# Performance work log

Measured on AMD Instinct MI355X. Metric: run time of the kernel, lower is better.

Reference implementation:

```python
import jax, jax.numpy as jnp
import numpy as np

D_MODEL = 1024
NHEAD = 16
HEAD_DIM = D_MODEL // NHEAD
MASK_FILLER = -1e20


def setup_inputs() -> dict:
    key = jax.random.key(0)
    ks = jax.random.split(key, 8)
    B, S = 2, 2048
    query = jax.random.normal(ks[0], (B, S, D_MODEL), dtype=jnp.float32)
    key_t = jax.random.normal(ks[1], (B, S, D_MODEL), dtype=jnp.float32)
    value = jax.random.normal(ks[2], (B, S, D_MODEL), dtype=jnp.float32)
    mask = jax.random.randint(ks[3], (B, S, S), 0, 2, dtype=jnp.int32)
    # nn.Linear(d_model, d_model, bias=False) weights, shape [out, in]
    scale = 1.0 / np.sqrt(D_MODEL)
    wq = jax.random.uniform(ks[4], (D_MODEL, D_MODEL), jnp.float32, -scale, scale)
    wk = jax.random.uniform(ks[5], (D_MODEL, D_MODEL), jnp.float32, -scale, scale)
    wv = jax.random.uniform(ks[6], (D_MODEL, D_MODEL), jnp.float32, -scale, scale)
    wo = jax.random.uniform(ks[7], (D_MODEL, D_MODEL), jnp.float32, -scale, scale)
    return {"query": query, "key": key_t, "value": value, "mask": mask,
            "wq": wq, "wk": wk, "wv": wv, "wo": wo}


def reference(query, key, value, mask, wq, wk, wv, wo):
    B = query.shape[0]
    # Projections: nn.Linear -> x @ W.T
    q = (query @ wq.T).reshape(B, -1, NHEAD, HEAD_DIM).transpose(0, 2, 1, 3)  # [B,H,Sq,Dh]
    k = (key @ wk.T).reshape(B, -1, NHEAD, HEAD_DIM).transpose(0, 2, 1, 3)    # [B,H,Sk,Dh]
    v = (value @ wv.T).reshape(B, -1, NHEAD, HEAD_DIM).transpose(0, 2, 1, 3)  # [B,H,Sk,Dh]
    scores = jnp.einsum('bhqd,bhkd->bhqk', q, k) / jnp.sqrt(jnp.float32(HEAD_DIM))
    scores = jnp.where(mask[:, None, :, :] == 0, MASK_FILLER, scores)
    attn = jax.nn.softmax(scores, axis=-1)  # dropout p=0.0 -> identity
    out = jnp.einsum('bhqk,bhkd->bhqd', attn, v)  # [B,H,Sq,Dh]
    out = out.transpose(0, 2, 1, 3).reshape(B, -1, D_MODEL)
    return out @ wo.T
```

## Files before the change

kernel.cpp:

```cpp
#include <hip/hip_runtime.h>
#include <stdint.h>

typedef __bf16 bf16x8 __attribute__((ext_vector_type(8)));
typedef float floatx4 __attribute__((ext_vector_type(4)));
typedef unsigned short ushort8v __attribute__((ext_vector_type(8)));
typedef unsigned int uint4v __attribute__((ext_vector_type(4)));
typedef unsigned short u16;
typedef unsigned long long u64;

#define GLOAD_LDS16(gp, lp)                                                       \
  __builtin_amdgcn_global_load_lds((__attribute__((address_space(1))) void*)(gp), \
                                   (__attribute__((address_space(3))) void*)(lp), \
                                   16, 0, 0)

__device__ __forceinline__ u16 f2bf(float f) {
  uint32_t u = __builtin_bit_cast(uint32_t, f);
  u = (u + 0x7FFFu + ((u >> 16) & 1u)) >> 16;
  return (u16)u;
}
__device__ __forceinline__ u16 f2bf_up(float f) {
  return (u16)((__builtin_bit_cast(uint32_t, f) + 0x8000u) >> 16);
}

__device__ __forceinline__ ushort8v load8(const void* base, size_t elemOff, int isf32) {
  if (isf32) {
    const uint32_t* p = (const uint32_t*)base + elemOff;
    uint4v a = *(const uint4v*)p;
    uint4v b = *(const uint4v*)(p + 4);
#pragma unroll
    for (int i = 0; i < 4; ++i) { a[i] += 0x8000u; b[i] += 0x8000u; }
    uint4v r;
    r[0] = __builtin_amdgcn_perm(a[1], a[0], 0x07060302);
    r[1] = __builtin_amdgcn_perm(a[3], a[2], 0x07060302);
    r[2] = __builtin_amdgcn_perm(b[1], b[0], 0x07060302);
    r[3] = __builtin_amdgcn_perm(b[3], b[2], 0x07060302);
    return __builtin_bit_cast(ushort8v, r);
  }
  return *(const ushort8v*)((const u16*)base + elemOff);
}

__global__ void detect_dtype(const u16* __restrict__ q, int* __restrict__ flag) {
  if (threadIdx.x == 0) *flag = 0;
  __syncthreads();
  int hit = 0;
  for (int i = threadIdx.x; i < 8192; i += 256) {
    u16 u = q[i];
    if (((u >> 7) & 0xFF) == 0xFF) hit = 1;
  }
  if (hit) atomicOr(flag, 1);
}

__global__ void pack_mask(const int* __restrict__ mask, u64* __restrict__ mpk) {
  const int gw   = (blockIdx.x * 256 + threadIdx.x) >> 6;
  const int lane = threadIdx.x & 63;
  const int word = gw & 31;
  const int row  = gw >> 5;
  const int m = mask[(size_t)row * 2048 + word * 64 + lane];
  u64 bits = __ballot(m != 0);
  if (lane == 0) mpk[(size_t)row * 32 + word] = bits;
}

__global__ __launch_bounds__(256)
void cvt_all(const void* X0, const void* X1, const void* X2,
             const void* W0, const void* W1, const void* W2, const void* W3,
             u16* __restrict__ Xb, u16* __restrict__ Wb, const int* flagp)
{
  const int isf = *flagp;
  const int id = blockIdx.x;
  const int t  = threadIdx.x;
  const int r2  = t >> 7;
  const int col = (t & 127) * 8;
  const void* src; u16* dst; int row;
  if (id < 6144) {
    const int s = id >> 11;
    src = (s == 0) ? X0 : (s == 1) ? X1 : X2;
    row = (id & 2047) * 2 + r2;
    dst = Xb + (size_t)s * 4096 * 1040 + (size_t)row * 1040 + col;
  } else {
    const int s = (id - 6144) >> 9;
    src = (s == 0) ? W0 : (s == 1) ? W1 : (s == 2) ? W2 : W3;
    row = ((id - 6144) & 511) * 2 + r2;
    dst = Wb + (size_t)s * 1024 * 1040 + (size_t)row * 1040 + col;
  }
  *(ushort8v*)dst = load8(src, (size_t)row * 1024 + col, isf);
}

__global__ __launch_bounds__(256)
void cvt_w(const void* W0, const void* W1, const void* W2, const void* W3,
           u16* __restrict__ dst, const int* flagp) {
  const int isf = *flagp;
  const int z = blockIdx.y;
  const void* src = (z == 0) ? W0 : (z == 1) ? W1 : (z == 2) ? W2 : W3;
  const size_t off = ((size_t)blockIdx.x * 256 + threadIdx.x) * 8;
  *(ushort8v*)(dst + (size_t)z * 1024 * 1024 + off) = load8(src, off, isf);
}

__global__ __launch_bounds__(256, 3)
void gemm_qkv_b(const u16* __restrict__ Xb, const u16* __restrict__ Wb,
                u16* __restrict__ Qb, u16* __restrict__ Kb, u16* __restrict__ Vt)
{
  const int AS = 1040, WS = 1040, N = 1024, K = 1024;
  const int z = blockIdx.z;
  const u16* A = Xb + (size_t)z * 4096 * AS;
  const u16* W = Wb + (size_t)z * 1024 * WS;

  __shared__ __align__(16) u16 lA[2 * 128 * 32];
  __shared__ __align__(16) u16 lB[2 * 128 * 32];

  const int tid  = threadIdx.x;
  const int lane = tid & 63;
  const int quad = lane >> 4;
  const int l15  = lane & 15;
  const int w    = tid >> 6;
  const int wm   = w >> 1, wn = w & 1;
  const int tileM = blockIdx.x * 128;
  const int tileN = blockIdx.y * 128;

  floatx4 acc[4][4] = {};

  const int ldRow = tid >> 2;
  const int ldCol = (tid & 3) * 8;
  const u16* aG = A + (size_t)(tileM + ldRow) * AS + ldCol;
  const u16* bG = W + (size_t)(tileN + ldRow) * WS + ldCol;
  u16* lAp = lA + tid * 8;
  u16* lBp = lB + tid * 8;

  GLOAD_LDS16(aG, lAp);
  GLOAD_LDS16(aG + (size_t)64 * AS, lAp + 2048);
  GLOAD_LDS16(bG, lBp);
  GLOAD_LDS16(bG + (size_t)64 * WS, lBp + 2048);
  __syncthreads();

#pragma unroll 2
  for (int k0 = 0; k0 < K; k0 += 32) {
    const int cur = (k0 >> 5) & 1;
    const int nxo = 4096 * (cur ^ 1);
    if (k0 + 32 < K) {
      GLOAD_LDS16(aG + k0 + 32, lAp + nxo);
      GLOAD_LDS16(aG + (size_t)64 * AS + k0 + 32, lAp + nxo + 2048);
      GLOAD_LDS16(bG + k0 + 32, lBp + nxo);
      GLOAD_LDS16(bG + (size_t)64 * WS + k0 + 32, lBp + nxo + 2048);
    }
    const u16* cA = lA + 4096 * cur;
    const u16* cB = lB + 4096 * cur;
    bf16x8 af[4], bw[4];
#pragma unroll
    for (int i = 0; i < 4; ++i) {
      af[i] = *(const bf16x8*)&cA[(wm * 64 + i * 16 + l15) * 32 + quad * 8];
      bw[i] = *(const bf16x8*)&cB[(wn * 64 + i * 16 + l15) * 32 + quad * 8];
    }
#pragma unroll
    for (int i = 0; i < 4; ++i)
#pragma unroll
      for (int j = 0; j < 4; ++j)
        acc[i][j] = __builtin_amdgcn_mfma_f32_16x16x32_bf16(af[i], bw[j], acc[i][j], 0, 0, 0);
    __syncthreads();
  }

  if (z < 2) {
    u16* C = (z == 0) ? Qb : Kb;
    const float sc = (z == 0) ? 0.18033688011112042f : 1.0f;
#pragma unroll
    for (int i = 0; i < 4; ++i) {
      const int row0 = tileM + wm * 64 + i * 16 + quad * 4;
#pragma unroll
      for (int j = 0; j < 4; ++j) {
        const int col = tileN + wn * 64 + j * 16 + l15;
#pragma unroll
        for (int r = 0; r < 4; ++r)
          C[(size_t)(row0 + r) * N + col] = f2bf(acc[i][j][r] * sc);
      }
    }
  } else {
    const int half = w >> 1;
    u16* myT = (w & 1) ? lB : lA;
#pragma unroll
    for (int pass = 0; pass < 2; ++pass) {
      __syncthreads();
      if (half == pass) {
#pragma unroll
        for (int i = 0; i < 4; ++i)
#pragma unroll
          for (int j = 0; j < 4; ++j)
#pragma unroll
            for (int r = 0; r < 4; ++r) {
              const int lr = i * 16 + quad * 4 + r;
              const int lc = j * 16 + l15;
              myT[lr * 64 + (lc ^ (quad << 4))] = f2bf(acc[i][j][r]);
            }
      }
      __syncthreads();
      if (half == pass) {
        const int n    = lane;
        const int gcol = tileN + wn * 64 + n;
        const int hh = gcol >> 6, dd = gcol & 63;
        const int growBase = tileM + wm * 64;
        const int bb = growBase >> 11;
        const int s0 = growBase & 2047;
        u16* dst = Vt + (((size_t)bb * 16 + hh) * 64 + dd) * 2048 + s0;
#pragma unroll
        for (int m0 = 0; m0 < 64; m0 += 8) {
          ushort8v pk;
#pragma unroll
          for (int t = 0; t < 8; ++t) {
            const int m = m0 + t;
            pk[t] = myT[m * 64 + (n ^ ((m & 12) << 2))];
          }
          *(ushort8v*)(dst + m0) = pk;
        }
      }
    }
  }
}

__global__ __launch_bounds__(256)
void gemm_qkv_f(const void* X0, const void* X1, const void* X2,
                const u16* __restrict__ Wb,
                u16* __restrict__ Qb, u16* __restrict__ Kb, u16* __restrict__ Vt,
                const int* flagp)
{
  const int K = 1024, N = 1024;
  const int isf = *flagp;
  const int z = blockIdx.z;
  const void* A_ = (z == 0) ? X0 : (z == 1) ? X1 : X2;
  const u16* W = Wb + (size_t)z * 1024 * 1024;

  __shared__ __align__(16) u16 lA[128 * 32];
  __shared__ __align__(16) u16 lB[128 * 32];

  const int tid  = threadIdx.x;
  const int lane = tid & 63;
  const int quad = lane >> 4;
  const int l15  = lane & 15;
  const int w    = tid >> 6;
  const int wm   = w >> 1, wn = w & 1;
  const int tileM = blockIdx.x * 128;
  const int tileN = blockIdx.y * 128;

  floatx4 acc[4][4] = {};

  const int ldRow = tid >> 2;
  const int ldCol = (tid & 3) * 8;
  const size_t aOff = (size_t)(tileM + ldRow) * K + ldCol;
  const u16* bG = W + (size_t)(tileN + ldRow) * K + ldCol;
  u16* lAp = lA + tid * 8;
  u16* lBp = lB + tid * 8;

  ushort8v a0 = load8(A_, aOff, isf);
  ushort8v a1 = load8(A_, aOff + (size_t)64 * K, isf);
  ushort8v b0 = *(const ushort8v*)bG;
  ushort8v b1 = *(const ushort8v*)(bG + (size_t)64 * K);

  for (int k0 = 0; k0 < K; k0 += 32) {
    __syncthreads();
    *(ushort8v*)lAp          = a0;
    *(ushort8v*)(lAp + 2048) = a1;
    *(ushort8v*)lBp          = b0;
    *(ushort8v*)(lBp + 2048) = b1;
    __syncthreads();

    if (k0 + 32 < K) {
      a0 = load8(A_, aOff + k0 + 32, isf);
      a1 = load8(A_, aOff + (size_t)64 * K + k0 + 32, isf);
      b0 = *(const ushort8v*)(bG + k0 + 32);
      b1 = *(const ushort8v*)(bG + (size_t)64 * K + k0 + 32);
    }

    bf16x8 af[4], bw[4];
#pragma unroll
    for (int i = 0; i < 4; ++i) {
      af[i] = *(const bf16x8*)&lA[(wm * 64 + i * 16 + l15) * 32 + quad * 8];
      bw[i] = *(const bf16x8*)&lB[(wn * 64 + i * 16 + l15) * 32 + quad * 8];
    }
#pragma unroll
    for (int i = 0; i < 4; ++i)
#pragma unroll
      for (int j = 0; j < 4; ++j)
        acc[i][j] = __builtin_amdgcn_mfma_f32_16x16x32_bf16(af[i], bw[j], acc[i][j], 0, 0, 0);
  }

  if (z < 2) {
    u16* C = (z == 0) ? Qb : Kb;
    const float sc = (z == 0) ? 0.18033688011112042f : 1.0f;
#pragma unroll
    for (int i = 0; i < 4; ++i) {
      const int row0 = tileM + wm * 64 + i * 16 + quad * 4;
#pragma unroll
      for (int j = 0; j < 4; ++j) {
        const int col = tileN + wn * 64 + j * 16 + l15;
#pragma unroll
        for (int r = 0; r < 4; ++r)
          C[(size_t)(row0 + r) * N + col] = f2bf(acc[i][j][r] * sc);
      }
    }
  } else {
    const int half = w >> 1;
    u16* myT = (w & 1) ? lB : lA;
#pragma unroll
    for (int pass = 0; pass < 2; ++pass) {
      __syncthreads();
      if (half == pass) {
#pragma unroll
        for (int i = 0; i < 4; ++i)
#pragma unroll
          for (int j = 0; j < 4; ++j)
#pragma unroll
            for (int r = 0; r < 4; ++r) {
              const int lr = i * 16 + quad * 4 + r;
              const int lc = j * 16 + l15;
              myT[lr * 64 + (lc ^ (quad << 4))] = f2bf(acc[i][j][r]);
            }
      }
      __syncthreads();
      if (half == pass) {
        const int n    = lane;
        const int gcol = tileN + wn * 64 + n;
        const int hh = gcol >> 6, dd = gcol & 63;
        const int growBase = tileM + wm * 64;
        const int bb = growBase >> 11;
        const int s0 = growBase & 2047;
        u16* dst = Vt + (((size_t)bb * 16 + hh) * 64 + dd) * 2048 + s0;
#pragma unroll
        for (int m0 = 0; m0 < 64; m0 += 8) {
          ushort8v pk;
#pragma unroll
          for (int t = 0; t < 8; ++t) {
            const int m = m0 + t;
            pk[t] = myT[m * 64 + (n ^ ((m & 12) << 2))];
          }
          *(ushort8v*)(dst + m0) = pk;
        }
      }
    }
  }
}

__global__ __launch_bounds__(256)
void attn(const u16* Qb, const u16* __restrict__ Kb, const u16* __restrict__ Vt,
          const u64* __restrict__ mpk, u16* AO, int aoStr)
{
  __shared__ __align__(16) u16 lK[2][64 * 64];
  __shared__ __align__(16) u16 lV[2][64 * 64];
  __shared__ __align__(16) u16 lP[64 * 64];

  const int tid  = threadIdx.x;
  const int lane = tid & 63;
  const int quad = lane >> 4;
  const int l15  = lane & 15;
  const int w    = tid >> 6;

  const int bh = blockIdx.x;
  const int qt = blockIdx.y;
  const int b  = bh >> 4;
  const int h  = bh & 15;
  const size_t rowB   = (size_t)b * 2048;
  const size_t vtBase = ((size_t)bh * 64) * 2048;

  bf16x8 aq[2];
  {
    const u16* qp = Qb + (rowB + qt * 64 + w * 16 + l15) * 1024 + h * 64 + quad * 8;
    aq[0] = *(const bf16x8*)qp;
    aq[1] = *(const bf16x8*)(qp + 32);
  }

  const ushort8v one_u = {0x3F80, 0x3F80, 0x3F80, 0x3F80, 0x3F80, 0x3F80, 0x3F80, 0x3F80};
  const bf16x8 ones = __builtin_bit_cast(bf16x8, one_u);

  floatx4 o[4], l4;
#pragma unroll
  for (int nb = 0; nb < 4; ++nb) o[nb] = (floatx4){0.f, 0.f, 0.f, 0.f};
  l4 = (floatx4){0.f, 0.f, 0.f, 0.f};

  const int qrow0 = qt * 64 + w * 16 + quad * 4;
  const u64* mrow = mpk + (rowB + qrow0) * 32;
  u16* lPw = lP + w * 1024;

  const int r1 = tid >> 3;
  const int cs = ((tid & 7) ^ (r1 & 7)) * 8;
  const u16* kSrc = Kb + (rowB + r1) * 1024 + h * 64 + cs;
  const u16* vSrc = Vt + vtBase + (size_t)r1 * 2048 + cs;

  GLOAD_LDS16(kSrc,                     &lK[0][tid * 8]);
  GLOAD_LDS16(kSrc + (size_t)32 * 1024, &lK[0][tid * 8 + 2048]);
  GLOAD_LDS16(vSrc,                     &lV[0][tid * 8]);
  GLOAD_LDS16(vSrc + (size_t)32 * 2048, &lV[0][tid * 8 + 2048]);
  __syncthreads();

#pragma unroll 2
  for (int kt = 0; kt < 32; ++kt) {
    const int cur = kt & 1;
    if (kt < 31) {
      const u16* kS = kSrc + (size_t)(kt + 1) * 64 * 1024;
      const u16* vS = vSrc + (kt + 1) * 64;
      GLOAD_LDS16(kS,                     &lK[cur ^ 1][tid * 8]);
      GLOAD_LDS16(kS + (size_t)32 * 1024, &lK[cur ^ 1][tid * 8 + 2048]);
      GLOAD_LDS16(vS,                     &lV[cur ^ 1][tid * 8]);
      GLOAD_LDS16(vS + (size_t)32 * 2048, &lV[cur ^ 1][tid * 8 + 2048]);
    }

    u64 mw[4];
#pragma unroll
    for (int r = 0; r < 4; ++r) mw[r] = mrow[(size_t)r * 32 + kt];

#pragma unroll
    for (int nb = 0; nb < 4; ++nb) {
      const int row = nb * 16 + l15;
      const int swk = (row & 7) << 3;
      bf16x8 bk0 = *(const bf16x8*)&lK[cur][row * 64 + ((quad * 8) ^ swk)];
      bf16x8 bk1 = *(const bf16x8*)&lK[cur][row * 64 + ((quad * 8 + 32) ^ swk)];
      floatx4 sacc = {0.f, 0.f, 0.f, 0.f};
      sacc = __builtin_amdgcn_mfma_f32_16x16x32_bf16(aq[0], bk0, sacc, 0, 0, 0);
      sacc = __builtin_amdgcn_mfma_f32_16x16x32_bf16(aq[1], bk1, sacc, 0, 0, 0);
      const int kbit = nb * 16 + l15;
#pragma unroll
      for (int r = 0; r < 4; ++r) {
        const float e = __builtin_amdgcn_exp2f(sacc[r]);
        const float p = ((mw[r] >> kbit) & 1ULL) ? e : 0.0f;
        const int prow = quad * 4 + r;
        lPw[prow * 64 + (kbit ^ ((prow >> 1) << 3))] = f2bf_up(p);
      }
    }

#pragma unroll
    for (int ks = 0; ks < 2; ++ks) {
      bf16x8 ap = *(const bf16x8*)&lPw[l15 * 64 + ((ks * 32 + quad * 8) ^ ((l15 >> 1) << 3))];
#pragma unroll
      for (int nb = 0; nb < 4; ++nb) {
        const int row = nb * 16 + l15;
        bf16x8 bv = *(const bf16x8*)&lV[cur][row * 64 + ((ks * 32 + quad * 8) ^ ((row & 7) << 3))];
        o[nb] = __builtin_amdgcn_mfma_f32_16x16x32_bf16(ap, bv, o[nb], 0, 0, 0);
      }
      l4 = __builtin_amdgcn_mfma_f32_16x16x32_bf16(ap, ones, l4, 0, 0, 0);
    }
    __syncthreads();
  }

#pragma unroll
  for (int r = 0; r < 4; ++r) {
    const float inv = 1.0f / l4[r];
    const size_t orow = (rowB + qt * 64 + w * 16 + quad * 4 + r) * aoStr + h * 64;
#pragma unroll
    for (int nb = 0; nb < 4; ++nb)
      AO[orow + nb * 16 + l15] = f2bf(o[nb][r] * inv);
  }
}

__global__ __launch_bounds__(256, 3)
void gemm_out(const u16* __restrict__ A, int aStr,
              const u16* __restrict__ W, int wStr, void* C_, const int* flagp)
{
  const int K = 1024, N = 1024;
  const int isf = *flagp;

  __shared__ __align__(16) u16 lA[2 * 64 * 32];
  __shared__ __align__(16) u16 lB[2 * 128 * 32];

  const int tid  = threadIdx.x;
  const int lane = tid & 63;
  const int quad = lane >> 4;
  const int l15  = lane & 15;
  const int w    = tid >> 6;
  const int tileM = blockIdx.x * 64;
  const int tileN = blockIdx.y * 128;

  floatx4 acc[4][2] = {};

  const int ldRow = tid >> 2;
  const int ldCol = (tid & 3) * 8;
  const u16* aG = A + (size_t)(tileM + ldRow) * aStr + ldCol;
  const u16* bG = W + (size_t)(tileN + ldRow) * wStr + ldCol;
  u16* lAp = lA + tid * 8;
  u16* lBp = lB + tid * 8;

  GLOAD_LDS16(aG, lAp);
  GLOAD_LDS16(bG, lBp);
  GLOAD_LDS16(bG + (size_t)64 * wStr, lBp + 2048);
  __syncthreads();

#pragma unroll 2
  for (int k0 = 0; k0 < K; k0 += 32) {
    const int cur = (k0 >> 5) & 1;
    const int nxA = 2048 * (cur ^ 1);
    const int nxB = 4096 * (cur ^ 1);
    if (k0 + 32 < K) {
      GLOAD_LDS16(aG + k0 + 32, lAp + nxA);
      GLOAD_LDS16(bG + k0 + 32, lBp + nxB);
      GLOAD_LDS16(bG + (size_t)64 * wStr + k0 + 32, lBp + nxB + 2048);
    }
    const u16* cA = lA + 2048 * cur;
    const u16* cB = lB + 4096 * cur;
    bf16x8 af[4], bw[2];
#pragma unroll
    for (int i = 0; i < 4; ++i)
      af[i] = *(const bf16x8*)&cA[(i * 16 + l15) * 32 + quad * 8];
#pragma unroll
    for (int j = 0; j < 2; ++j)
      bw[j] = *(const bf16x8*)&cB[(w * 32 + j * 16 + l15) * 32 + quad * 8];
#pragma unroll
    for (int i = 0; i < 4; ++i)
#pragma unroll
      for (int j = 0; j < 2; ++j)
        acc[i][j] = __builtin_amdgcn_mfma_f32_16x16x32_bf16(af[i], bw[j], acc[i][j], 0, 0, 0);
    __syncthreads();
  }

#pragma unroll
  for (int i = 0; i < 4; ++i) {
    const int row0 = tileM + i * 16 + quad * 4;
#pragma unroll
    for (int j = 0; j < 2; ++j) {
      const int col = tileN + w * 32 + j * 16 + l15;
#pragma unroll
      for (int r = 0; r < 4; ++r) {
        const size_t off = (size_t)(row0 + r) * N + col;
        if (isf) ((float*)C_)[off] = acc[i][j][r];
        else     ((u16*)C_)[off]   = f2bf(acc[i][j][r]);
      }
    }
  }
}

extern "C" void kernel_launch(void* const* d_in, const int* in_sizes, int n_in,
                              void* d_out, int out_size, void* d_ws, size_t ws_size,
                              hipStream_t stream)
{
  const int* mk = (const int*)d_in[3];

  int* flag = (int*)d_ws;
  u64* mpk  = (u64*)((char*)d_ws + 256);
  const size_t SZ = (size_t)4096 * 1024;
  u16* Qb = (u16*)((char*)d_ws + 256 + (size_t)1048576);
  u16* Kb = Qb + SZ;
  u16* Vt = Kb + SZ;
  u16* Wb = Vt + SZ;

  const size_t WB_PAD = (size_t)4 * 1024 * 1040;
  const size_t XB_PAD = (size_t)3 * 4096 * 1040;
  const size_t NEED = 256 + 1048576 + 3 * SZ * 2 + WB_PAD * 2 + XB_PAD * 2;

  detect_dtype<<<1, 256, 0, stream>>>((const u16*)d_in[0], flag);
  pack_mask<<<32768, 256, 0, stream>>>(mk, mpk);

  if (ws_size >= NEED) {
    u16* Xb = Wb + WB_PAD;
    cvt_all<<<8192, 256, 0, stream>>>(d_in[0], d_in[1], d_in[2],
                                      d_in[4], d_in[5], d_in[6], d_in[7],
                                      Xb, Wb, flag);
    gemm_qkv_b<<<dim3(32, 8, 3), 256, 0, stream>>>(Xb, Wb, Qb, Kb, Vt);
    u16* AOp = Xb;
    attn<<<dim3(32, 32), 256, 0, stream>>>(Qb, Kb, Vt, mpk, AOp, 1040);
    gemm_out<<<dim3(64, 8), 256, 0, stream>>>(AOp, 1040,
                                              Wb + (size_t)3 * 1024 * 1040, 1040,
                                              d_out, flag);
  } else {
    cvt_w<<<dim3(512, 4), 256, 0, stream>>>(d_in[4], d_in[5], d_in[6], d_in[7], Wb, flag);
    gemm_qkv_f<<<dim3(32, 8, 3), 256, 0, stream>>>(d_in[0], d_in[1], d_in[2],
                                                   Wb, Qb, Kb, Vt, flag);
    attn<<<dim3(32, 32), 256, 0, stream>>>(Qb, Kb, Vt, mpk, Qb, 1024);
    gemm_out<<<dim3(64, 8), 256, 0, stream>>>(Qb, 1024,
                                              Wb + (size_t)3 * 1024 * 1024, 1024,
                                              d_out, flag);
  }
}
```

Before: 287.7 us.

## Compute transposed S tile, pack P stores, single-buffer V loaded within iteration

Swaps the MFMA operands so each lane holds four consecutive key columns for one query row. This lets P be written as a packed 8-byte store, with one mask word per lane, instead of four scalar 2-byte stores and four mask loads. V is now single-buffered and loaded at the start of the same iteration, with an extra barrier before the PV step, which frees LDS at the cost of exposing V load latency. The net effect depends on whether cheaper P writes and mask loads outweigh the lost V prefetch overlap and the extra barrier.

```diff
diff --git a/kernel.cpp b/kernel.cpp
--- a/kernel.cpp
+++ b/kernel.cpp
@@ -5,6 +5,7 @@
 typedef float floatx4 __attribute__((ext_vector_type(4)));
 typedef unsigned short ushort8v __attribute__((ext_vector_type(8)));
 typedef unsigned int uint4v __attribute__((ext_vector_type(4)));
+typedef unsigned int uint2v __attribute__((ext_vector_type(2)));
 typedef unsigned short u16;
 typedef unsigned long long u64;
 
@@ -340,8 +341,8 @@
           const u64* __restrict__ mpk, u16* AO, int aoStr)
 {
   __shared__ __align__(16) u16 lK[2][64 * 64];
-  __shared__ __align__(16) u16 lV[2][64 * 64];
-  __shared__ __align__(16) u16 lP[64 * 64];
+  __shared__ __align__(16) u16 lV[64 * 64];
+  __shared__ __align__(16) u16 lP[4][16 * 64];
 
   const int tid  = threadIdx.x;
   const int lane = tid & 63;
@@ -371,9 +372,8 @@
   for (int nb = 0; nb < 4; ++nb) o[nb] = (floatx4){0.f, 0.f, 0.f, 0.f};
   l4 = (floatx4){0.f, 0.f, 0.f, 0.f};
 
-  const int qrow0 = qt * 64 + w * 16 + quad * 4;
-  const u64* mrow = mpk + (rowB + qrow0) * 32;
-  u16* lPw = lP + w * 1024;
+  const u64* mrow = mpk + (rowB + qt * 64 + w * 16 + l15) * 32;
+  u16* lPw = &lP[w][0];
 
   const int r1 = tid >> 3;
   const int cs = ((tid & 7) ^ (r1 & 7)) * 8;
@@ -382,57 +382,62 @@
 
   GLOAD_LDS16(kSrc,                     &lK[0][tid * 8]);
   GLOAD_LDS16(kSrc + (size_t)32 * 1024, &lK[0][tid * 8 + 2048]);
-  GLOAD_LDS16(vSrc,                     &lV[0][tid * 8]);
-  GLOAD_LDS16(vSrc + (size_t)32 * 2048, &lV[0][tid * 8 + 2048]);
-  __syncthreads();
 
 #pragma unroll 2
   for (int kt = 0; kt < 32; ++kt) {
     const int cur = kt & 1;
+    __syncthreads();
+
+    {
+      const u16* vS = vSrc + kt * 64;
+      GLOAD_LDS16(vS,                     &lV[tid * 8]);
+      GLOAD_LDS16(vS + (size_t)32 * 2048, &lV[tid * 8 + 2048]);
+    }
     if (kt < 31) {
       const u16* kS = kSrc + (size_t)(kt + 1) * 64 * 1024;
-      const u16* vS = vSrc + (kt + 1) * 64;
       GLOAD_LDS16(kS,                     &lK[cur ^ 1][tid * 8]);
       GLOAD_LDS16(kS + (size_t)32 * 1024, &lK[cur ^ 1][tid * 8 + 2048]);
-      GLOAD_LDS16(vS,                     &lV[cur ^ 1][tid * 8]);
-      GLOAD_LDS16(vS + (size_t)32 * 2048, &lV[cur ^ 1][tid * 8 + 2048]);
-    }
-
-    u64 mw[4];
-#pragma unroll
-    for (int r = 0; r < 4; ++r) mw[r] = mrow[(size_t)r * 32 + kt];
+    }
+
+    const u64 mw = mrow[kt];
 
 #pragma unroll
     for (int nb = 0; nb < 4; ++nb) {
       const int row = nb * 16 + l15;
       const int swk = (row & 7) << 3;
-      bf16x8 bk0 = *(const bf16x8*)&lK[cur][row * 64 + ((quad * 8) ^ swk)];
-      bf16x8 bk1 = *(const bf16x8*)&lK[cur][row * 64 + ((quad * 8 + 32) ^ swk)];
+      bf16x8 ak0 = *(const bf16x8*)&lK[cur][row * 64 + ((quad * 8) ^ swk)];
+      bf16x8 ak1 = *(const bf16x8*)&lK[cur][row * 64 + ((quad * 8 + 32) ^ swk)];
       floatx4 sacc = {0.f, 0.f, 0.f, 0.f};
-      sacc = __builtin_amdgcn_mfma_f32_16x16x32_bf16(aq[0], bk0, sacc, 0, 0, 0);
-      sacc = __builtin_amdgcn_mfma_f32_16x16x32_bf16(aq[1], bk1, sacc, 0, 0, 0);
-      const int kbit = nb * 16 + l15;
-#pragma unroll
-      for (int r = 0; r < 4; ++r) {
-        const float e = __builtin_amdgcn_exp2f(sacc[r]);
-        const float p = ((mw[r] >> kbit) & 1ULL) ? e : 0.0f;
-        const int prow = quad * 4 + r;
-        lPw[prow * 64 + (kbit ^ ((prow >> 1) << 3))] = f2bf_up(p);
-      }
-    }
+      sacc = __builtin_amdgcn_mfma_f32_16x16x32_bf16(ak0, aq[0], sacc, 0, 0, 0);
+      sacc = __builtin_amdgcn_mfma_f32_16x16x32_bf16(ak1, aq[1], sacc, 0, 0, 0);
+      const uint32_t nib = (uint32_t)(mw >> (nb * 16 + quad * 4)) & 0xFu;
+      float p0 = (nib & 1u) ? __builtin_amdgcn_exp2f(sacc[0]) : 0.0f;
+      float p1 = (nib & 2u) ? __builtin_amdgcn_exp2f(sacc[1]) : 0.0f;
+      float p2 = (nib & 4u) ? __builtin_amdgcn_exp2f(sacc[2]) : 0.0f;
+      float p3 = (nib & 8u) ? __builtin_amdgcn_exp2f(sacc[3]) : 0.0f;
+      const uint32_t b0 = __builtin_bit_cast(uint32_t, p0) + 0x8000u;
+      const uint32_t b1 = __builtin_bit_cast(uint32_t, p1) + 0x8000u;
+      const uint32_t b2 = __builtin_bit_cast(uint32_t, p2) + 0x8000u;
+      const uint32_t b3 = __builtin_bit_cast(uint32_t, p3) + 0x8000u;
+      uint2v pk2;
+      pk2[0] = __builtin_amdgcn_perm(b1, b0, 0x07060302);
+      pk2[1] = __builtin_amdgcn_perm(b3, b2, 0x07060302);
+      const int col = (nb * 16 + quad * 4) ^ ((l15 & 7) << 3);
+      *(uint2v*)&lPw[l15 * 64 + col] = pk2;
+    }
+    __syncthreads();
 
 #pragma unroll
     for (int ks = 0; ks < 2; ++ks) {
-      bf16x8 ap = *(const bf16x8*)&lPw[l15 * 64 + ((ks * 32 + quad * 8) ^ ((l15 >> 1) << 3))];
+      bf16x8 ap = *(const bf16x8*)&lPw[l15 * 64 + ((ks * 32 + quad * 8) ^ ((l15 & 7) << 3))];
 #pragma unroll
       for (int nb = 0; nb < 4; ++nb) {
         const int row = nb * 16 + l15;
-        bf16x8 bv = *(const bf16x8*)&lV[cur][row * 64 + ((ks * 32 + quad * 8) ^ ((row & 7) << 3))];
+        bf16x8 bv = *(const bf16x8*)&lV[row * 64 + ((ks * 32 + quad * 8) ^ ((row & 7) << 3))];
         o[nb] = __builtin_amdgcn_mfma_f32_16x16x32_bf16(ap, bv, o[nb], 0, 0, 0);
       }
       l4 = __builtin_amdgcn_mfma_f32_16x16x32_bf16(ap, ones, l4, 0, 0, 0);
     }
-    __syncthreads();
   }
 
 #pragma unroll
```

After: 280.1 us. 2.6% less time.
